# Performance work log

Measured on AMD Instinct MI355X. Metric: run time of the kernel, lower is better.

Reference implementation:

```python
import jax, jax.numpy as jnp
import numpy as np

BITS, NF, NX = 8, 4096, 1024
G = NX // 8  # groups of 8 weights packed per uint8


def setup_inputs() -> dict:
    key = jax.random.key(0)
    k1, k2, k3, k4 = jax.random.split(key, 4)
    x = jax.random.normal(k1, (2, 2048, NX), dtype=jnp.float32)
    # packed sign bytes per (bit-plane, out-feature, group-of-8 inputs)
    binary = jax.random.randint(k2, (BITS, NF, G), 0, 256, dtype=jnp.int32)
    # per-bit-plane, per-output-row scale (always positive in the sup/l2 schemes)
    scale = jax.random.uniform(k3, (BITS, NF, 1), dtype=jnp.float32)
    bias = jax.random.normal(k4, (NF,), dtype=jnp.float32)
    return {"x": x, "binary": binary, "scale": scale, "bias": bias}


def _decode_signs(binary):
    # binary_exp in the torch code is [2^7..2^0], so element j of each group of 8
    # is stored in bit (7 - j). map4 maps a set bit -> +1, clear bit -> -1.
    shifts = jnp.arange(7, -1, -1, dtype=binary.dtype)
    bits = (binary[..., None] >> shifts) & 1  # (BITS, NF, G, 8)
    sign = jnp.where(bits == 1, 1.0, -1.0).astype(jnp.float32)
    return sign.reshape(binary.shape[0], binary.shape[1], -1)  # (BITS, NF, NX)


def reference(x, binary, scale, bias):
    # Math of the original forward:
    #   table[t, g, hi, lo] = x[t, 8g:8g+4] . map4[:, hi] + x[t, 8g+4:8g+8] . map4[:, lo]
    #   out[t, f] = sum_i scale[i, f] * sum_g table[t, g, binary[i,f,g]>>4, binary[i,f,g]&15]
    # which is exactly sum_i scale[i,f] * (x[t] . sign_i[f]).  We fold the
    # bit-plane sum into an effective weight and run one dense GEMM.
    size_out = x.shape[:-1] + (scale.shape[1],)
    xf = x.reshape(-1, x.shape[-1])            # (T, NX)
    sign = _decode_signs(binary)               # (BITS, NF, NX), values in {-1,+1}
    W = jnp.einsum('kfn,kfo->fn', sign, scale)  # effective weight (NF, NX)
    out = xf @ W.T + bias                      # (T, NF)
    return out.reshape(size_out)
```

## Files before the change

kernel.cpp:

```cpp
#include <hip/hip_runtime.h>
#include <hip/hip_bf16.h>
#include <stdint.h>


#define BITS 8
#define NF   4096
#define NXX  1024
#define GRP  (NXX / 8)

#define BM 256
#define BN 256
#define BK 64
#define NTHR 512

typedef __attribute__((ext_vector_type(4))) float f32x4;
typedef __attribute__((ext_vector_type(8))) short bf16x8;

__global__ __launch_bounds__(256) void k_prep(const float* __restrict__ x,
                                              const int* __restrict__ binary,
                                              const float* __restrict__ scale,
                                              __hip_bfloat16* __restrict__ xb,
                                              __hip_bfloat16* __restrict__ Wb) {
    const int b = blockIdx.x;
    const int tid = threadIdx.x;
    if (b < 2048) {
        int i = b * 256 + tid;
        const float4* xp = (const float4*)x;
        float4 a = xp[2 * i], c = xp[2 * i + 1];
        union { __hip_bfloat16 h[8]; int4 v; } u;
        u.h[0] = __float2bfloat16(a.x);
        u.h[1] = __float2bfloat16(a.y);
        u.h[2] = __float2bfloat16(a.z);
        u.h[3] = __float2bfloat16(a.w);
        u.h[4] = __float2bfloat16(c.x);
        u.h[5] = __float2bfloat16(c.y);
        u.h[6] = __float2bfloat16(c.z);
        u.h[7] = __float2bfloat16(c.w);
        ((int4*)xb)[i] = u.v;
    } else {
        int idx = (b - 2048) * 256 + tid;
        int f = idx >> 7;
        int g = idx & (GRP - 1);
        float sc[BITS];
        int   bv[BITS];
#pragma unroll
        for (int k = 0; k < BITS; ++k) {
            sc[k] = scale[k * NF + f];
            bv[k] = binary[(size_t)(k * NF + f) * GRP + g];
        }
        union { __hip_bfloat16 h[8]; int4 v; } u;
#pragma unroll
        for (int j = 0; j < 8; ++j) {
            float s = 0.f;
#pragma unroll
            for (int k = 0; k < BITS; ++k)
                s += ((bv[k] >> (7 - j)) & 1) ? sc[k] : -sc[k];
            u.h[j] = __float2bfloat16(s);
        }
        ((int4*)Wb)[idx] = u.v;
    }
}

__global__ __launch_bounds__(NTHR, 2) void k_gemm(const __hip_bfloat16* __restrict__ A,
                                                  const __hip_bfloat16* __restrict__ B,
                                                  const float* __restrict__ bias,
                                                  float* __restrict__ C,
                                                  int M, int N, int K) {
    __shared__ __align__(16) char lds[131072];

    const int tid  = threadIdx.x;
    const int lane = tid & 63;
    const int wid  = tid >> 6;
    const int wm = wid >> 2;
    const int wn = wid & 3;
    const int lr = lane & 15;
    const int lk = lane >> 4;

    const int nwg = gridDim.x;
    const int cpx = nwg >> 3;
    const int bid = blockIdx.x;
    const int swz = (bid & 7) * cpx + (bid >> 3);
    const int m0 = (swz >> 4) * BM;
    const int n0 = (swz & 15) * BN;

    const int NT = K / BK;
    const int NI = NT / 2;

    auto stage_unit = [&](int buf, int kt, int kind) {
        const bool isA = (kind < 2);
        const __hip_bfloat16* src = (isA ? A + (size_t)m0 * K : B + (size_t)n0 * K) + kt;
        char* base = lds + buf * 65536 + (isA ? 0 : 32768);
        int lrr = tid >> 3;
        int q   = tid & 7;
        int R0;
        if (isA) R0 = ((kind == 1) ? 64 : 0) + lrr;
        else     R0 = ((kind == 3) ? 32 : 0) + (lrr & 31) + ((lrr & 32) << 1);
#pragma unroll
        for (int call = 0; call < 2; ++call) {
            int R  = R0 + call * 128;
            int qs = q ^ (R & 7);
            __builtin_amdgcn_global_load_lds(
                (const __attribute__((address_space(1))) void*)(src + (size_t)R * K + qs * 8),
                (__attribute__((address_space(3))) void*)(base + R * 128 + q * 16), 16, 0, 0);
        }
    };
    auto ldA = [&](int buf, int msub, int i, int kk) -> bf16x8 {
        int R = wm * 128 + msub * 64 + i * 16 + lr;
        int CB = (kk * 64 + lk * 16) ^ ((R & 7) << 4);
        return *(const bf16x8*)(lds + buf * 65536 + R * 128 + CB);
    };
    auto ldB = [&](int buf, int nsub, int j, int kk) -> bf16x8 {
        int R = wn * 64 + nsub * 32 + j * 16 + lr;
        int CB = (kk * 64 + lk * 16) ^ ((R & 7) << 4);
        return *(const bf16x8*)(lds + buf * 65536 + 32768 + R * 128 + CB);
    };

    f32x4 acc[8][4] = {};
    bf16x8 aF[4][2], bF0[2][2], bF1[2][2];

#define BAR()   __builtin_amdgcn_s_barrier()
#define LGKM0() do { asm volatile("s_waitcnt lgkmcnt(0)" ::: "memory"); \
                     __builtin_amdgcn_sched_barrier(0); } while (0)
#define VM6()   do { __builtin_amdgcn_sched_barrier(0); \
                     asm volatile("s_waitcnt vmcnt(6)" ::: "memory"); } while (0)
#define PRIO1() __builtin_amdgcn_s_setprio(1)
#define PRIO0() do { __builtin_amdgcn_s_setprio(0); \
                     __builtin_amdgcn_sched_barrier(0); } while (0)
#define MFMA_Q(ms, ns, BF)                                                         \
    do {                                                                           \
        _Pragma("unroll") for (int i = 0; i < 4; ++i)                              \
        _Pragma("unroll") for (int j = 0; j < 2; ++j)                              \
        _Pragma("unroll") for (int kk = 0; kk < 2; ++kk)                           \
            acc[(ms)*4 + i][(ns)*2 + j] = __builtin_amdgcn_mfma_f32_16x16x32_bf16( \
                aF[i][kk], BF[j][kk], acc[(ms)*4 + i][(ns)*2 + j], 0, 0, 0);       \
    } while (0)

    stage_unit(0, 0, 0); stage_unit(0, 0, 2); stage_unit(0, 0, 3); stage_unit(0, 0, 1);
    stage_unit(1, BK, 2); stage_unit(1, BK, 3); stage_unit(1, BK, 1);
    asm volatile("s_waitcnt vmcnt(6)" ::: "memory");
    BAR();

    for (int it = 0; it < NI; ++it) {
        const int to = 2 * it + 1;
        const int tn = 2 * it + 2;
        const bool st = (it + 1 < NI);

#pragma unroll
        for (int i = 0; i < 4; ++i) { aF[i][0] = ldA(0, 0, i, 0); aF[i][1] = ldA(0, 0, i, 1); }
#pragma unroll
        for (int j = 0; j < 2; ++j) { bF0[j][0] = ldB(0, 0, j, 0); bF0[j][1] = ldB(0, 0, j, 1); }
        stage_unit(1, to * BK, 0);
        BAR(); LGKM0(); PRIO1(); MFMA_Q(0, 0, bF0); PRIO0(); BAR();

#pragma unroll
        for (int j = 0; j < 2; ++j) { bF1[j][0] = ldB(0, 1, j, 0); bF1[j][1] = ldB(0, 1, j, 1); }
        if (st) stage_unit(0, tn * BK, 2);
        BAR(); LGKM0(); PRIO1(); MFMA_Q(0, 1, bF1); PRIO0(); BAR();

#pragma unroll
        for (int i = 0; i < 4; ++i) { aF[i][0] = ldA(0, 1, i, 0); aF[i][1] = ldA(0, 1, i, 1); }
        if (st) stage_unit(0, tn * BK, 3);
        BAR(); LGKM0(); PRIO1(); MFMA_Q(1, 0, bF0); PRIO0(); BAR();

        if (st) stage_unit(0, tn * BK, 1);
        BAR(); PRIO1(); MFMA_Q(1, 1, bF1); PRIO0(); VM6(); BAR();

#pragma unroll
        for (int i = 0; i < 4; ++i) { aF[i][0] = ldA(1, 0, i, 0); aF[i][1] = ldA(1, 0, i, 1); }
#pragma unroll
        for (int j = 0; j < 2; ++j) { bF0[j][0] = ldB(1, 0, j, 0); bF0[j][1] = ldB(1, 0, j, 1); }
        if (st) stage_unit(0, tn * BK, 0);
        BAR(); LGKM0(); PRIO1(); MFMA_Q(0, 0, bF0); PRIO0(); BAR();

#pragma unroll
        for (int j = 0; j < 2; ++j) { bF1[j][0] = ldB(1, 1, j, 0); bF1[j][1] = ldB(1, 1, j, 1); }
        if (st) stage_unit(1, (tn + 1) * BK, 2);
        BAR(); LGKM0(); PRIO1(); MFMA_Q(0, 1, bF1); PRIO0(); BAR();

#pragma unroll
        for (int i = 0; i < 4; ++i) { aF[i][0] = ldA(1, 1, i, 0); aF[i][1] = ldA(1, 1, i, 1); }
        if (st) stage_unit(1, (tn + 1) * BK, 3);
        BAR(); LGKM0(); PRIO1(); MFMA_Q(1, 0, bF0); PRIO0(); BAR();

        if (st) stage_unit(1, (tn + 1) * BK, 1);
        BAR(); PRIO1(); MFMA_Q(1, 1, bF1); PRIO0(); VM6(); BAR();
    }

#undef BAR
#undef LGKM0
#undef VM6
#undef PRIO1
#undef PRIO0
#undef MFMA_Q

#pragma unroll
    for (int j = 0; j < 4; ++j) {
        int col = n0 + wn * 64 + j * 16 + lr;
        float bv = bias[col];
#pragma unroll
        for (int i = 0; i < 8; ++i) {
            int row = m0 + wm * 128 + i * 16 + lk * 4;
#pragma unroll
            for (int r = 0; r < 4; ++r)
                C[(size_t)(row + r) * N + col] = acc[i][j][r] + bv;
        }
    }
}

extern "C" void kernel_launch(void* const* d_in, const int* in_sizes, int n_in,
                              void* d_out, int out_size, void* d_ws, size_t ws_size,
                              hipStream_t stream) {
    const float* x      = (const float*)d_in[0];
    const int*   binary = (const int*)d_in[1];
    const float* scale  = (const float*)d_in[2];
    const float* bias   = (const float*)d_in[3];
    float* out = (float*)d_out;

    const int M = in_sizes[0] / NXX;

    __hip_bfloat16* xb = (__hip_bfloat16*)d_ws;
    __hip_bfloat16* Wb = xb + (size_t)M * NXX;

    k_prep<<<2048 + (NF * GRP) / 256, 256, 0, stream>>>(x, binary, scale, xb, Wb);
    k_gemm<<<(M / BM) * (NF / BN), NTHR, 0, stream>>>(xb, Wb, bias, out, M, NF, NXX);
}
```

Baseline: 133.1 us.

## Restructure GEMM main loop into finer-grained per-tile pipeline with smaller fragment sets

Replaces the two-tile unrolled loop with a single-tile loop that splits each 128-row warp tile into four 32-row quarters. The quarters use two A fragment sets and two B fragment sets, and global-to-LDS stages are re-timed across phases with explicit vmcnt waits. The goal is to reduce register pressure from the A fragments and to overlap LDS reads and global loads with MFMA work at finer granularity. The trade-off is more barriers per K tile and a more fragile waitcnt schedule, which could stall or cause race hazards.

```diff
diff --git a/kernel.cpp b/kernel.cpp
--- a/kernel.cpp
+++ b/kernel.cpp
@@ -84,7 +84,6 @@
     const int n0 = (swz & 15) * BN;
 
     const int NT = K / BK;
-    const int NI = NT / 2;
 
     auto stage_unit = [&](int buf, int kt, int kind) {
         const bool isA = (kind < 2);
@@ -104,94 +103,99 @@
                 (__attribute__((address_space(3))) void*)(base + R * 128 + q * 16), 16, 0, 0);
         }
     };
-    auto ldA = [&](int buf, int msub, int i, int kk) -> bf16x8 {
-        int R = wm * 128 + msub * 64 + i * 16 + lr;
+    auto ldA = [&](int buf, int qr, int i, int kk) -> bf16x8 {
+        int R = wm * 128 + qr * 32 + i * 16 + lr;
         int CB = (kk * 64 + lk * 16) ^ ((R & 7) << 4);
         return *(const bf16x8*)(lds + buf * 65536 + R * 128 + CB);
     };
-    auto ldB = [&](int buf, int nsub, int j, int kk) -> bf16x8 {
-        int R = wn * 64 + nsub * 32 + j * 16 + lr;
+    auto ldB = [&](int buf, int ns, int j, int kk) -> bf16x8 {
+        int R = wn * 64 + ns * 32 + j * 16 + lr;
         int CB = (kk * 64 + lk * 16) ^ ((R & 7) << 4);
         return *(const bf16x8*)(lds + buf * 65536 + 32768 + R * 128 + CB);
     };
 
     f32x4 acc[8][4] = {};
-    bf16x8 aF[4][2], bF0[2][2], bF1[2][2];
+    bf16x8 aS0[2][2], aS1[2][2], bF0[2][2], bF1[2][2];
 
 #define BAR()   __builtin_amdgcn_s_barrier()
-#define LGKM0() do { asm volatile("s_waitcnt lgkmcnt(0)" ::: "memory"); \
-                     __builtin_amdgcn_sched_barrier(0); } while (0)
-#define VM6()   do { __builtin_amdgcn_sched_barrier(0); \
-                     asm volatile("s_waitcnt vmcnt(6)" ::: "memory"); } while (0)
+#define SB0()   __builtin_amdgcn_sched_barrier(0)
+#define LGKM0() do { asm volatile("s_waitcnt lgkmcnt(0)" ::: "memory"); SB0(); } while (0)
 #define PRIO1() __builtin_amdgcn_s_setprio(1)
-#define PRIO0() do { __builtin_amdgcn_s_setprio(0); \
-                     __builtin_amdgcn_sched_barrier(0); } while (0)
-#define MFMA_Q(ms, ns, BF)                                                         \
+#define PRIO0() do { __builtin_amdgcn_s_setprio(0); SB0(); } while (0)
+#define LDA2(D, b, qr) do { \
+    D[0][0] = ldA(b, qr, 0, 0); D[0][1] = ldA(b, qr, 0, 1); \
+    D[1][0] = ldA(b, qr, 1, 0); D[1][1] = ldA(b, qr, 1, 1); } while (0)
+#define LDB2(D, b, ns) do { \
+    D[0][0] = ldB(b, ns, 0, 0); D[0][1] = ldB(b, ns, 0, 1); \
+    D[1][0] = ldB(b, ns, 1, 0); D[1][1] = ldB(b, ns, 1, 1); } while (0)
+#define QUAD(mq, nq, AS, BF)                                                       \
     do {                                                                           \
-        _Pragma("unroll") for (int i = 0; i < 4; ++i)                              \
+        _Pragma("unroll") for (int i = 0; i < 2; ++i)                              \
         _Pragma("unroll") for (int j = 0; j < 2; ++j)                              \
         _Pragma("unroll") for (int kk = 0; kk < 2; ++kk)                           \
-            acc[(ms)*4 + i][(ns)*2 + j] = __builtin_amdgcn_mfma_f32_16x16x32_bf16( \
-                aF[i][kk], BF[j][kk], acc[(ms)*4 + i][(ns)*2 + j], 0, 0, 0);       \
+            acc[(mq)*2 + i][(nq)*2 + j] = __builtin_amdgcn_mfma_f32_16x16x32_bf16( \
+                AS[i][kk], BF[j][kk], acc[(mq)*2 + i][(nq)*2 + j], 0, 0, 0);       \
     } while (0)
 
-    stage_unit(0, 0, 0); stage_unit(0, 0, 2); stage_unit(0, 0, 3); stage_unit(0, 0, 1);
-    stage_unit(1, BK, 2); stage_unit(1, BK, 3); stage_unit(1, BK, 1);
-    asm volatile("s_waitcnt vmcnt(6)" ::: "memory");
-    BAR();
-
-    for (int it = 0; it < NI; ++it) {
-        const int to = 2 * it + 1;
-        const int tn = 2 * it + 2;
-        const bool st = (it + 1 < NI);
-
-#pragma unroll
-        for (int i = 0; i < 4; ++i) { aF[i][0] = ldA(0, 0, i, 0); aF[i][1] = ldA(0, 0, i, 1); }
-#pragma unroll
-        for (int j = 0; j < 2; ++j) { bF0[j][0] = ldB(0, 0, j, 0); bF0[j][1] = ldB(0, 0, j, 1); }
-        stage_unit(1, to * BK, 0);
-        BAR(); LGKM0(); PRIO1(); MFMA_Q(0, 0, bF0); PRIO0(); BAR();
-
-#pragma unroll
-        for (int j = 0; j < 2; ++j) { bF1[j][0] = ldB(0, 1, j, 0); bF1[j][1] = ldB(0, 1, j, 1); }
-        if (st) stage_unit(0, tn * BK, 2);
-        BAR(); LGKM0(); PRIO1(); MFMA_Q(0, 1, bF1); PRIO0(); BAR();
-
-#pragma unroll
-        for (int i = 0; i < 4; ++i) { aF[i][0] = ldA(0, 1, i, 0); aF[i][1] = ldA(0, 1, i, 1); }
-        if (st) stage_unit(0, tn * BK, 3);
-        BAR(); LGKM0(); PRIO1(); MFMA_Q(1, 0, bF0); PRIO0(); BAR();
-
-        if (st) stage_unit(0, tn * BK, 1);
-        BAR(); PRIO1(); MFMA_Q(1, 1, bF1); PRIO0(); VM6(); BAR();
-
-#pragma unroll
-        for (int i = 0; i < 4; ++i) { aF[i][0] = ldA(1, 0, i, 0); aF[i][1] = ldA(1, 0, i, 1); }
-#pragma unroll
-        for (int j = 0; j < 2; ++j) { bF0[j][0] = ldB(1, 0, j, 0); bF0[j][1] = ldB(1, 0, j, 1); }
-        if (st) stage_unit(0, tn * BK, 0);
-        BAR(); LGKM0(); PRIO1(); MFMA_Q(0, 0, bF0); PRIO0(); BAR();
-
-#pragma unroll
-        for (int j = 0; j < 2; ++j) { bF1[j][0] = ldB(1, 1, j, 0); bF1[j][1] = ldB(1, 1, j, 1); }
-        if (st) stage_unit(1, (tn + 1) * BK, 2);
-        BAR(); LGKM0(); PRIO1(); MFMA_Q(0, 1, bF1); PRIO0(); BAR();
-
-#pragma unroll
-        for (int i = 0; i < 4; ++i) { aF[i][0] = ldA(1, 1, i, 0); aF[i][1] = ldA(1, 1, i, 1); }
-        if (st) stage_unit(1, (tn + 1) * BK, 3);
-        BAR(); LGKM0(); PRIO1(); MFMA_Q(1, 0, bF0); PRIO0(); BAR();
-
-        if (st) stage_unit(1, (tn + 1) * BK, 1);
-        BAR(); PRIO1(); MFMA_Q(1, 1, bF1); PRIO0(); VM6(); BAR();
+    stage_unit(0, 0, 0);
+    stage_unit(0, 0, 2);
+    stage_unit(0, 0, 1);
+    stage_unit(0, 0, 3);
+    stage_unit(1, BK, 0);
+    stage_unit(1, BK, 2);
+    asm volatile("s_waitcnt vmcnt(8)" ::: "memory");
+    BAR(); SB0();
+
+    for (int t = 0; t < NT; ++t) {
+        const int b = t & 1;
+        const int o = b ^ 1;
+
+        LDA2(aS0, b, 0);
+        LDB2(bF0, b, 0);
+        if (t <= NT - 2) stage_unit(o, (t + 1) * BK, 1);
+        BAR(); LGKM0();
+        PRIO1(); QUAD(0, 0, aS0, bF0); PRIO0();
+        if (t < NT - 1) { asm volatile("s_waitcnt vmcnt(6)" ::: "memory"); }
+        else            { asm volatile("s_waitcnt vmcnt(0)" ::: "memory"); }
+        BAR(); SB0();
+
+        LDB2(bF1, b, 1);
+        if (t <= NT - 2) stage_unit(o, (t + 1) * BK, 3);
+        BAR(); LGKM0();
+        PRIO1(); QUAD(0, 1, aS0, bF1); PRIO0();
+
+        LDA2(aS1, b, 1);
+        BAR(); LGKM0();
+        PRIO1(); QUAD(1, 0, aS1, bF0); PRIO0();
+
+        BAR();
+        PRIO1(); QUAD(1, 1, aS1, bF1); PRIO0();
+
+        LDA2(aS0, b, 2);
+        if (t <= NT - 3) stage_unit(b, (t + 2) * BK, 0);
+        BAR(); LGKM0();
+        PRIO1(); QUAD(2, 0, aS0, bF0); QUAD(2, 1, aS0, bF1); PRIO0();
+
+        LDA2(aS1, b, 3);
+        BAR(); LGKM0();
+        PRIO1(); QUAD(3, 0, aS1, bF0); PRIO0();
+
+        if (t <= NT - 3) stage_unit(b, (t + 2) * BK, 2);
+        BAR();
+        PRIO1(); QUAD(3, 1, aS1, bF1); PRIO0();
+        if (t <= NT - 3)      { asm volatile("s_waitcnt vmcnt(8)" ::: "memory"); }
+        else if (t == NT - 2) { asm volatile("s_waitcnt vmcnt(4)" ::: "memory"); }
+        BAR(); SB0();
     }
 
 #undef BAR
+#undef SB0
 #undef LGKM0
-#undef VM6
 #undef PRIO1
 #undef PRIO0
-#undef MFMA_Q
+#undef LDA2
+#undef LDB2
+#undef QUAD
 
 #pragma unroll
     for (int j = 0; j < 4; ++j) {
```

New measurement: 131.1 us. No clear change (-1.5%).
